# Kernel optimization log

Hardware: AMD Instinct MI355X
Metric: run time of the kernel (lower is better)

The kernel has to match this reference:

```python
import jax, jax.numpy as jnp
import numpy as np

H = 1024
B = 8
S = 2048

def setup_inputs() -> dict:
    key = jax.random.key(0)
    ks = jax.random.split(key, 16)
    w = lambda k, shp: (jax.random.normal(k, shp, dtype=jnp.float32) * 0.02)
    return {
        "hidden_states": jax.random.normal(ks[0], (B, S, H), dtype=jnp.float32),
        "context_vector": jax.random.normal(ks[1], (B, H), dtype=jnp.float32),
        # nn.Linear weights stored torch-style as [out, in]
        "Wq": w(ks[2], (H, H)), "bq": w(ks[3], (H,)),
        "Wk": w(ks[4], (H, H)), "bk": w(ks[5], (H,)),
        "Wv": w(ks[6], (H, H)), "bv": w(ks[7], (H,)),
        "Wcq": w(ks[8], (H, H)),  # only .weight.t() used in original (no bias)
        "Wck": w(ks[9], (H, H)),
        "g_qh": jax.random.normal(ks[10], (H, 1), dtype=jnp.float32),
        "g_kh": jax.random.normal(ks[11], (H, 1), dtype=jnp.float32),
        "g_qc": jax.random.normal(ks[12], (H, 1), dtype=jnp.float32),
        "g_kc": jax.random.normal(ks[13], (H, 1), dtype=jnp.float32),
    }

def reference(hidden_states, context_vector, Wq, bq, Wk, bk, Wv, bv, Wcq, Wck, g_qh, g_kh, g_qc, g_kc):
    # Linear projections (torch Linear: x @ W.T + b)
    query = jnp.einsum('bsh,oh->bso', hidden_states, Wq) + bq   # [B,S,H]
    key_  = jnp.einsum('bsh,oh->bso', hidden_states, Wk) + bk
    value = jnp.einsum('bsh,oh->bso', hidden_states, Wv) + bv

    # gate = sigmoid(Q @ g_h + (ctx @ g_c)[:,None,:])  -> [B,S,1]
    q_gate = jax.nn.sigmoid(query @ g_qh + (context_vector @ g_qc)[:, None, :])
    k_gate = jax.nn.sigmoid(key_  @ g_kh + (context_vector @ g_kc)[:, None, :])

    # context projections: ctx @ weight.t() (no bias in original usage) -> [B,1,H]
    ctx_q = (context_vector @ Wcq.T)[:, None, :]
    ctx_k = (context_vector @ Wck.T)[:, None, :]

    query_hat = (1.0 - q_gate) * query + q_gate * ctx_q
    key_hat   = (1.0 - k_gate) * key_  + k_gate * ctx_k

    scale = 1.0 / jnp.sqrt(jnp.asarray(H, dtype=jnp.float32))
    scores = jnp.einsum('bqh,bkh->bqk', query_hat, key_hat) * scale  # [B,S,S]
    probs = jax.nn.softmax(scores, axis=-1)
    output = jnp.einsum('bqk,bkh->bqh', probs, value)  # [B,S,H]
    return (output, scores)
```

## Files before the change

kernel.cpp:

```cpp
#include <hip/hip_runtime.h>
#include <cstdint>
#include <cstddef>

#define H 1024
#define NB 8
#define S 2048
#define MROWS (NB*S)

using short8  = __attribute__((ext_vector_type(8))) short;
using ushort8 = __attribute__((ext_vector_type(8))) unsigned short;
using f32x4   = __attribute__((ext_vector_type(4))) float;

__device__ __forceinline__ unsigned short f2bf(float f){
  union { float f; unsigned int u; } c; c.f = f;
  unsigned int u = c.u;
  return (unsigned short)((u + 0x7fffu + ((u >> 16) & 1u)) >> 16);
}
__device__ __forceinline__ float bf2f(unsigned short b){
  union { unsigned int u; float f; } c; c.u = ((unsigned int)b) << 16;
  return c.f;
}

__global__ __launch_bounds__(256) void k_prep(
    const float* __restrict__ Wq, const float* __restrict__ Wk, const float* __restrict__ Wv,
    const float* __restrict__ Wcq, const float* __restrict__ Wck, const float* __restrict__ ctx,
    const float* __restrict__ gqh, const float* __restrict__ gkh,
    const float* __restrict__ bq, const float* __restrict__ bk,
    const float* __restrict__ gqc, const float* __restrict__ gkc,
    unsigned short* __restrict__ wqb, unsigned short* __restrict__ wkb, unsigned short* __restrict__ wvb,
    float* __restrict__ up, float* __restrict__ ctxq, float* __restrict__ ctxk,
    float* __restrict__ scal)
{
  __shared__ float cs[NB * H];
  const int bid = blockIdx.x;
  const int t = threadIdx.x;
  if (bid < 3072){
    const int y = bid >> 10;
    const int x = bid & 1023;
    const float* src = y == 0 ? Wq : (y == 1 ? Wk : Wv);
    unsigned short* dst = y == 0 ? wqb : (y == 1 ? wkb : wvb);
    const int i = (x * 256 + t) * 4;
    float4 v = *reinterpret_cast<const float4*>(src + i);
    ushort4 o; o.x = f2bf(v.x); o.y = f2bf(v.y); o.z = f2bf(v.z); o.w = f2bf(v.w);
    *reinterpret_cast<ushort4*>(dst + i) = o;
  } else if (bid < 3136){
    const int sub = bid - 3072;
    const int z = sub >> 5;
    const int y = (sub >> 2) & 7;
    const int x = sub & 3;
    const float* W = z ? Wk : Wq;
    const float* g = z ? gkh : gqh;
    const int in = x * 256 + t;
    const int o0 = y * 128;
    float s = 0.f;
    for (int o = 0; o < 128; ++o) s = fmaf(W[(size_t)(o0 + o) * H + in], g[o0 + o], s);
    up[(z * 8 + y) * 1024 + in] = s;
  } else if (bid < 3648){
    const int sub = bid - 3136;
    const int y = sub >> 8;
    const int x = sub & 255;
    const float* W = y ? Wck : Wcq;
    float* out = y ? ctxk : ctxq;
    for (int i = t; i < NB * H; i += 256) cs[i] = ctx[i];
    __syncthreads();
    const int wid = t >> 6, lane = t & 63;
    const int row = x * 4 + wid;
    float a[NB];
    #pragma unroll
    for (int b = 0; b < NB; ++b) a[b] = 0.f;
    for (int i0 = 0; i0 < H; i0 += 64){
      const float w = W[(size_t)row * H + i0 + lane];
      #pragma unroll
      for (int b = 0; b < NB; ++b) a[b] = fmaf(w, cs[b * H + i0 + lane], a[b]);
    }
    #pragma unroll
    for (int b = 0; b < NB; ++b){
      float v = a[b];
      #pragma unroll
      for (int off = 32; off > 0; off >>= 1) v += __shfl_xor(v, off);
      if (lane == 0) out[b * H + row] = v;
    }
  } else {
    const int wid = t >> 6, lane = t & 63;
    for (int d = wid; d < 18; d += 4){
      const float *pa, *pb;
      if (d == 0){ pa = bq; pb = gqh; }
      else if (d == 1){ pa = bk; pb = gkh; }
      else if (d < 10){ pa = ctx + (d - 2) * H; pb = gqc; }
      else { pa = ctx + (d - 10) * H; pb = gkc; }
      float s = 0.f;
      for (int i = lane; i < H; i += 64) s = fmaf(pa[i], pb[i], s);
      #pragma unroll
      for (int off = 32; off > 0; off >>= 1) s += __shfl_xor(s, off);
      if (lane == 0) scal[d] = s;
    }
  }
}

__global__ void k_ucombine(const float* __restrict__ up, float* __restrict__ u2){
  int i = blockIdx.x * 256 + threadIdx.x;
  int z = i >> 10, h = i & 1023;
  float s = 0.f;
  #pragma unroll
  for (int c = 0; c < 8; ++c) s += up[(z * 8 + c) * 1024 + h];
  u2[i] = s;
}

__global__ __launch_bounds__(256) void k_prepass(const float* __restrict__ hs,
    const float* __restrict__ u2, const float* __restrict__ scal,
    unsigned short* __restrict__ hsb, float* __restrict__ gq, float* __restrict__ gk){
  const int t = threadIdx.x, wid = t >> 6, lane = t & 63;
  const int row = blockIdx.x * 4 + wid;
  const float* hrow = hs + (size_t)row * H;
  const float* u_q = u2;
  const float* u_k = u2 + 1024;
  unsigned short* orow = hsb + (size_t)row * H;
  float sq = 0.f, sk = 0.f;
  #pragma unroll
  for (int c = 0; c < 4; ++c){
    const int idx = (lane + c * 64) * 4;
    float4 v  = *reinterpret_cast<const float4*>(hrow + idx);
    float4 uq = *reinterpret_cast<const float4*>(u_q + idx);
    float4 uk = *reinterpret_cast<const float4*>(u_k + idx);
    ushort4 o; o.x = f2bf(v.x); o.y = f2bf(v.y); o.z = f2bf(v.z); o.w = f2bf(v.w);
    *reinterpret_cast<ushort4*>(orow + idx) = o;
    sq += v.x*uq.x + v.y*uq.y + v.z*uq.z + v.w*uq.w;
    sk += v.x*uk.x + v.y*uk.y + v.z*uk.z + v.w*uk.w;
  }
  #pragma unroll
  for (int off = 32; off > 0; off >>= 1){
    sq += __shfl_xor(sq, off);
    sk += __shfl_xor(sk, off);
  }
  if (lane == 0){
    const int b = row >> 11;
    gq[row] = 1.f / (1.f + __expf(-(sq + scal[0] + scal[2 + b])));
    gk[row] = 1.f / (1.f + __expf(-(sk + scal[1] + scal[10 + b])));
  }
}


#define STG(bufi, opi, halfi, koff, P0, P1) \
  do { __builtin_amdgcn_global_load_lds((const __attribute__((address_space(1))) void*)(P0 + (koff)), \
      (__attribute__((address_space(3))) void*)((char*)(&lds[bufi][opi][halfi][0]) + (wid*2+0)*1024), 16, 0, 0); \
    __builtin_amdgcn_global_load_lds((const __attribute__((address_space(1))) void*)(P1 + (koff)), \
      (__attribute__((address_space(3))) void*)((char*)(&lds[bufi][opi][halfi][0]) + (wid*2+1)*1024), 16, 0, 0); } while(0)
#define STG_A(bufi, halfi, koff) STG(bufi, 0, halfi, koff, sA0, sA1)
#define STG_B(bufi, halfi, koff) STG(bufi, 1, halfi, koff, sB0, sB1)

#define DS_A(bufi, ks, mh) \
  do { _Pragma("unroll") for (int m_ = 0; m_ < 4; ++m_){ \
      const int ar_ = wr*128 + ((mh)*4 + m_)*16 + (lane & 15); \
      const int sl_ = (lane >> 4) ^ ((ar_ >> 1) & 3); \
      af[m_] = *reinterpret_cast<const short8*>(&lds[bufi][0][ks][ar_*32 + sl_*8]); } } while(0)
#define DS_B(bufi, ks) \
  do { _Pragma("unroll") for (int n_ = 0; n_ < 4; ++n_){ \
      const int br_ = wc*64 + n_*16 + (lane & 15); \
      const int sl_ = (lane >> 4) ^ ((br_ >> 1) & 3); \
      bf[n_] = *reinterpret_cast<const short8*>(&lds[bufi][1][ks][br_*32 + sl_*8]); } } while(0)
#define MFMA16(mh) \
  do { __builtin_amdgcn_s_setprio(1); \
    _Pragma("unroll") for (int m_ = 0; m_ < 4; ++m_) \
      _Pragma("unroll") for (int n_ = 0; n_ < 4; ++n_) \
        acc[(mh)*4 + m_][n_] = __builtin_amdgcn_mfma_f32_16x16x32_bf16(af[m_], bf[n_], acc[(mh)*4 + m_][n_], 0, 0, 0); \
    __builtin_amdgcn_s_setprio(0); } while(0)
#define VM4() do { asm volatile("s_waitcnt vmcnt(4)" ::: "memory"); } while(0)
#define VM0() do { asm volatile("s_waitcnt vmcnt(0)" ::: "memory"); } while(0)
#define BAR() do { asm volatile("" ::: "memory"); __builtin_amdgcn_s_barrier(); asm volatile("" ::: "memory"); } while(0)

template<int MODE>
__global__ __launch_bounds__(512, 2)
void k_gemm(const unsigned short* __restrict__ A, const unsigned short* __restrict__ B,
            int K, int ldA, int ldB, long long Abatch, long long Bbatch,
            const float* __restrict__ gq, const float* __restrict__ gk,
            const float* __restrict__ bq, const float* __restrict__ bk, const float* __restrict__ bv,
            const float* __restrict__ cq, const float* __restrict__ ck,
            unsigned short* __restrict__ oq, unsigned short* __restrict__ ok, unsigned short* __restrict__ ov,
            float* __restrict__ outf, long long outBatch, float scale, float* __restrict__ rsum)
{
  __shared__ __align__(16) short lds[2][2][2][8192];

  const int t = threadIdx.x;
  const int wid = t >> 6, lane = t & 63;
  const int wr = wid >> 2, wc = wid & 3;
  const int bz = blockIdx.z;
  const unsigned short* Ab = A + (size_t)bz * (size_t)Abatch;
  const unsigned short* Bb = B + (size_t)bz * (size_t)Bbatch;
  const int row0 = blockIdx.x * 256;
  const int col0 = blockIdx.y * 256;

  const int c0 = (wid*2 + 0)*64 + lane;
  const int c1 = (wid*2 + 1)*64 + lane;
  const int r0s = c0 >> 2, r1s = c1 >> 2;
  const int kc0 = (c0 & 3) ^ ((r0s >> 1) & 3);
  const int kc1 = (c1 & 3) ^ ((r1s >> 1) & 3);
  const unsigned short* sA0 = Ab + (size_t)(row0 + r0s) * (size_t)ldA + kc0*8;
  const unsigned short* sA1 = Ab + (size_t)(row0 + r1s) * (size_t)ldA + kc1*8;
  const unsigned short* sB0 = Bb + (size_t)(col0 + r0s) * (size_t)ldB + kc0*8;
  const unsigned short* sB1 = Bb + (size_t)(col0 + r1s) * (size_t)ldB + kc1*8;

  f32x4 acc[8][4] = {};
  short8 af[4], bf[4];

  STG_A(0, 0, 0); STG_B(0, 0, 0); STG_A(0, 1, 32); STG_B(0, 1, 32);
  VM0(); BAR();

  const int niter = K >> 7;
  for (int it = 0; it < niter; ++it){
    const int t1k = (it*2 + 1) << 6;
    const int t2k = (it*2 + 2) << 6;
    const bool more = (it + 1 < niter);
    DS_A(0, 0, 0); DS_B(0, 0); STG_A(1, 0, t1k);      MFMA16(0);                              BAR();
    DS_A(0, 0, 1);             STG_B(1, 0, t1k);      MFMA16(1); VM4();                       BAR();
    DS_A(0, 1, 0); DS_B(0, 1); STG_A(1, 1, t1k + 32); MFMA16(0);                              BAR();
    DS_A(0, 1, 1);             STG_B(1, 1, t1k + 32); MFMA16(1); if (more) { VM4(); } else { VM0(); } BAR();
    DS_A(1, 0, 0); DS_B(1, 0); if (more) { STG_A(0, 0, t2k); }      MFMA16(0);                BAR();
    DS_A(1, 0, 1);             if (more) { STG_B(0, 0, t2k); }      MFMA16(1); if (more) { VM4(); } BAR();
    DS_A(1, 1, 0); DS_B(1, 1); if (more) { STG_A(0, 1, t2k + 32); } MFMA16(0);                BAR();
    DS_A(1, 1, 1);             if (more) { STG_B(0, 1, t2k + 32); } MFMA16(1); if (more) { VM4(); } BAR();
  }

  if constexpr (MODE == 0){
    const int which = col0 >> 10;
    const int lcol  = col0 & 1023;
    if (which < 2){
      const float* gate = which ? gk : gq;
      const float* bias = which ? bk : bq;
      const float* ctxv = which ? ck : cq;
      unsigned short* outb = which ? ok : oq;
      unsigned short* tp = (unsigned short*)lds;
      float* gl = (float*)((char*)lds + 69632);
      float* bl = gl + 256;
      float* cl = bl + 256;
      const int b = row0 >> 11;
      __syncthreads();
      if (t < 256){
        gl[t] = gate[row0 + t];
        bl[t] = bias[lcol + t];
        cl[t] = ctxv[b * H + lcol + t];
      }
      __syncthreads();
      #pragma unroll
      for (int ci = 0; ci < 2; ++ci){
        if (ci) __syncthreads();
        if (wr == ci){
          #pragma unroll
          for (int mi = 0; mi < 8; ++mi)
            #pragma unroll
            for (int r = 0; r < 4; ++r){
              const int lr = mi*16 + (lane >> 4)*4 + r;
              const float g = gl[ci*128 + lr];
              #pragma unroll
              for (int n = 0; n < 4; ++n){
                const int lc = wc*64 + n*16 + (lane & 15);
                const float q = acc[mi][n][r] + bl[lc];
                tp[lr*264 + lc] = f2bf((1.f - g) * q + g * cl[lc]);
              }
            }
        }
        __syncthreads();
        const int rr = t & 127;
        const int cc = (t >> 7) * 64;
        const unsigned short* srcp = tp + rr*264 + cc;
        unsigned short* dst = outb + (size_t)(row0 + ci*128 + rr) * H + lcol + cc;
        #pragma unroll
        for (int i = 0; i < 64; i += 8)
          *reinterpret_cast<ushort8*>(dst + i) = *reinterpret_cast<const ushort8*>(srcp + i);
      }
    } else {
      unsigned short* tp = (unsigned short*)lds;
      const int bb = row0 >> 11;
      const int s0 = row0 & (S - 1);
      #pragma unroll
      for (int ci = 0; ci < 2; ++ci)
        #pragma unroll
        for (int cj = 0; cj < 2; ++cj){
          __syncthreads();
          if (wr == ci && (wc >> 1) == cj){
            const int lc0 = (wc & 1) * 64;
            #pragma unroll
            for (int mi = 0; mi < 8; ++mi)
              #pragma unroll
              for (int n = 0; n < 4; ++n)
                #pragma unroll
                for (int r = 0; r < 4; ++r){
                  const int lr = mi*16 + (lane >> 4)*4 + r;
                  const int lc = lc0 + n*16 + (lane & 15);
                  tp[lc*136 + lr] = f2bf(acc[mi][n][r] + bv[lcol + cj*128 + lc]);
                }
          }
          __syncthreads();
          const int hh = t & 127;
          const int sc = (t >> 7) * 32;
          const unsigned short* srcp = tp + hh*136 + sc;
          unsigned short* vout = ov + (size_t)bb * H * S + (size_t)(lcol + cj*128 + hh) * S
                                    + (size_t)(s0 + ci*128 + sc);
          #pragma unroll
          for (int i2 = 0; i2 < 32; i2 += 8)
            *reinterpret_cast<ushort8*>(vout + i2) = *reinterpret_cast<const ushort8*>(srcp + i2);
        }
    }
  } else if constexpr (MODE == 3){
    float* rowacc = (float*)lds;
    __syncthreads();
    if (t < 256) rowacc[t] = 0.f;
    __syncthreads();
    #pragma unroll
    for (int mi = 0; mi < 8; ++mi)
      #pragma unroll
      for (int r = 0; r < 4; ++r){
        const int lr = wr*128 + mi*16 + (lane >> 4)*4 + r;
        const int grow = row0 + lr;
        float psum = 0.f;
        #pragma unroll
        for (int n = 0; n < 4; ++n){
          const int gcol = col0 + wc*64 + n*16 + (lane & 15);
          const float val = acc[mi][n][r] * scale;
          outf[(size_t)bz * (size_t)outBatch + (size_t)grow * S + gcol] = val;
          const float pe = __expf(fminf(val, 80.f));
          const unsigned short pb = f2bf(pe);
          oq[(size_t)bz * (size_t)outBatch + (size_t)grow * S + gcol] = pb;
          psum += bf2f(pb);
        }
        #pragma unroll
        for (int off = 1; off < 16; off <<= 1) psum += __shfl_xor(psum, off);
        if ((lane & 15) == 0) atomicAdd(&rowacc[lr], psum);
      }
    __syncthreads();
    if (t < 256) atomicAdd(&rsum[bz * S + row0 + t], rowacc[t]);
  } else {
    float* rs = (float*)lds;
    __syncthreads();
    if (t < 256) rs[t] = 1.f / fmaxf(rsum[bz * S + row0 + t], 1e-35f);
    __syncthreads();
    #pragma unroll
    for (int mi = 0; mi < 8; ++mi)
      #pragma unroll
      for (int r = 0; r < 4; ++r){
        const int lr = wr*128 + mi*16 + (lane >> 4)*4 + r;
        const float inv = rs[lr];
        #pragma unroll
        for (int n = 0; n < 4; ++n){
          const int gcol = col0 + wc*64 + n*16 + (lane & 15);
          outf[(size_t)bz * (size_t)outBatch + (size_t)(row0 + lr) * H + gcol] = acc[mi][n][r] * inv;
        }
      }
  }
}

extern "C" void kernel_launch(void* const* d_in, const int* in_sizes, int n_in,
                              void* d_out, int out_size, void* d_ws, size_t ws_size,
                              hipStream_t stream) {
  const float* hs  = (const float*)d_in[0];
  const float* ctx = (const float*)d_in[1];
  const float* Wq  = (const float*)d_in[2];
  const float* bq  = (const float*)d_in[3];
  const float* Wk  = (const float*)d_in[4];
  const float* bk  = (const float*)d_in[5];
  const float* Wv  = (const float*)d_in[6];
  const float* bv  = (const float*)d_in[7];
  const float* Wcq = (const float*)d_in[8];
  const float* Wck = (const float*)d_in[9];
  const float* gqh = (const float*)d_in[10];
  const float* gkh = (const float*)d_in[11];
  const float* gqc = (const float*)d_in[12];
  const float* gkc = (const float*)d_in[13];

  char* ws = (char*)d_ws;
  unsigned short* hsb   = (unsigned short*)(ws);
  unsigned short* qhat  = (unsigned short*)(ws + 33554432);
  unsigned short* khat  = (unsigned short*)(ws + 67108864);
  unsigned short* vt    = (unsigned short*)(ws + 100663296);
  unsigned short* probs = (unsigned short*)(ws + 134217728);
  unsigned short* wqb   = (unsigned short*)(ws + 201326592);
  unsigned short* wkb   = (unsigned short*)(ws + 203423744);
  unsigned short* wvb   = (unsigned short*)(ws + 205520896);
  float* up    = (float*)(ws + 207618048);
  float* u2    = (float*)(ws + 207683584);
  float* ctxq  = (float*)(ws + 207691776);
  float* ctxk  = (float*)(ws + 207724544);
  float* gq    = (float*)(ws + 207757312);
  float* gk    = (float*)(ws + 207822848);
  float* scal  = (float*)(ws + 207888384);
  float* rsum  = (float*)(ws + 207888640);

  float* out_attn   = (float*)d_out;
  float* out_scores = out_attn + (size_t)MROWS * H;

  hipMemsetAsync(rsum, 0, MROWS * sizeof(float), stream);

  k_prep<<<3649, 256, 0, stream>>>(Wq, Wk, Wv, Wcq, Wck, ctx, gqh, gkh, bq, bk, gqc, gkc,
      wqb, wkb, wvb, up, ctxq, ctxk, scal);
  k_ucombine<<<8, 256, 0, stream>>>(up, u2);
  k_prepass<<<MROWS / 4, 256, 0, stream>>>(hs, u2, scal, hsb, gq, gk);

  k_gemm<0><<<dim3(64, 12, 1), 512, 0, stream>>>(hsb, wqb, 1024, 1024, 1024, 0, 0,
      gq, gk, bq, bk, bv, ctxq, ctxk, qhat, khat, vt, nullptr, 0, 1.f, nullptr);

  k_gemm<3><<<dim3(8, 8, 8), 512, 0, stream>>>(qhat, khat, 1024, 1024, 1024,
      (long long)S * H, (long long)S * H,
      nullptr, nullptr, nullptr, nullptr, nullptr, nullptr, nullptr,
      probs, nullptr, nullptr, out_scores, (long long)S * S, 0.03125f, rsum);

  k_gemm<5><<<dim3(8, 4, 8), 512, 0, stream>>>(probs, vt, 2048, 2048, 2048,
      (long long)S * S, (long long)H * S,
      nullptr, nullptr, nullptr, nullptr, nullptr, nullptr, nullptr,
      nullptr, nullptr, nullptr, out_attn, (long long)S * H, 1.f, rsum);
}
```

Before: 327.6 us.

## Shrink GEMM tiles to 128x128 with 256 threads and single-buffered LDS

Replaces the 256x256-tile, 512-thread, double-buffered software-pipelined GEMM with a 128x128-tile, 256-thread kernel. The new kernel loads a 64-wide K slice per iteration, waits, then computes. It uses less LDS and fewer registers so three blocks can fit per CU, and launches four times as many blocks. In exchange it loses the overlap between global-to-LDS loads and MFMA work, and it halves operand reuse per tile, which raises global and L2 traffic. The epilogues are simplified to match the smaller tile.

```diff
diff --git a/kernel.cpp b/kernel.cpp
--- a/kernel.cpp
+++ b/kernel.cpp
@@ -140,36 +140,11 @@
 }
 
 
-#define STG(bufi, opi, halfi, koff, P0, P1) \
-  do { __builtin_amdgcn_global_load_lds((const __attribute__((address_space(1))) void*)(P0 + (koff)), \
-      (__attribute__((address_space(3))) void*)((char*)(&lds[bufi][opi][halfi][0]) + (wid*2+0)*1024), 16, 0, 0); \
-    __builtin_amdgcn_global_load_lds((const __attribute__((address_space(1))) void*)(P1 + (koff)), \
-      (__attribute__((address_space(3))) void*)((char*)(&lds[bufi][opi][halfi][0]) + (wid*2+1)*1024), 16, 0, 0); } while(0)
-#define STG_A(bufi, halfi, koff) STG(bufi, 0, halfi, koff, sA0, sA1)
-#define STG_B(bufi, halfi, koff) STG(bufi, 1, halfi, koff, sB0, sB1)
-
-#define DS_A(bufi, ks, mh) \
-  do { _Pragma("unroll") for (int m_ = 0; m_ < 4; ++m_){ \
-      const int ar_ = wr*128 + ((mh)*4 + m_)*16 + (lane & 15); \
-      const int sl_ = (lane >> 4) ^ ((ar_ >> 1) & 3); \
-      af[m_] = *reinterpret_cast<const short8*>(&lds[bufi][0][ks][ar_*32 + sl_*8]); } } while(0)
-#define DS_B(bufi, ks) \
-  do { _Pragma("unroll") for (int n_ = 0; n_ < 4; ++n_){ \
-      const int br_ = wc*64 + n_*16 + (lane & 15); \
-      const int sl_ = (lane >> 4) ^ ((br_ >> 1) & 3); \
-      bf[n_] = *reinterpret_cast<const short8*>(&lds[bufi][1][ks][br_*32 + sl_*8]); } } while(0)
-#define MFMA16(mh) \
-  do { __builtin_amdgcn_s_setprio(1); \
-    _Pragma("unroll") for (int m_ = 0; m_ < 4; ++m_) \
-      _Pragma("unroll") for (int n_ = 0; n_ < 4; ++n_) \
-        acc[(mh)*4 + m_][n_] = __builtin_amdgcn_mfma_f32_16x16x32_bf16(af[m_], bf[n_], acc[(mh)*4 + m_][n_], 0, 0, 0); \
-    __builtin_amdgcn_s_setprio(0); } while(0)
-#define VM4() do { asm volatile("s_waitcnt vmcnt(4)" ::: "memory"); } while(0)
 #define VM0() do { asm volatile("s_waitcnt vmcnt(0)" ::: "memory"); } while(0)
 #define BAR() do { asm volatile("" ::: "memory"); __builtin_amdgcn_s_barrier(); asm volatile("" ::: "memory"); } while(0)
 
 template<int MODE>
-__global__ __launch_bounds__(512, 2)
+__global__ __launch_bounds__(256, 3)
 void k_gemm(const unsigned short* __restrict__ A, const unsigned short* __restrict__ B,
             int K, int ldA, int ldB, long long Abatch, long long Bbatch,
             const float* __restrict__ gq, const float* __restrict__ gk,
@@ -178,46 +153,69 @@
             unsigned short* __restrict__ oq, unsigned short* __restrict__ ok, unsigned short* __restrict__ ov,
             float* __restrict__ outf, long long outBatch, float scale, float* __restrict__ rsum)
 {
-  __shared__ __align__(16) short lds[2][2][2][8192];
+  __shared__ __align__(16) short lds[20480];
+  short* As = lds;
+  short* Bs = lds + 8192;
 
   const int t = threadIdx.x;
   const int wid = t >> 6, lane = t & 63;
-  const int wr = wid >> 2, wc = wid & 3;
+  const int wr = wid >> 1, wc = wid & 1;
   const int bz = blockIdx.z;
   const unsigned short* Ab = A + (size_t)bz * (size_t)Abatch;
   const unsigned short* Bb = B + (size_t)bz * (size_t)Bbatch;
-  const int row0 = blockIdx.x * 256;
-  const int col0 = blockIdx.y * 256;
-
-  const int c0 = (wid*2 + 0)*64 + lane;
-  const int c1 = (wid*2 + 1)*64 + lane;
-  const int r0s = c0 >> 2, r1s = c1 >> 2;
-  const int kc0 = (c0 & 3) ^ ((r0s >> 1) & 3);
-  const int kc1 = (c1 & 3) ^ ((r1s >> 1) & 3);
-  const unsigned short* sA0 = Ab + (size_t)(row0 + r0s) * (size_t)ldA + kc0*8;
-  const unsigned short* sA1 = Ab + (size_t)(row0 + r1s) * (size_t)ldA + kc1*8;
-  const unsigned short* sB0 = Bb + (size_t)(col0 + r0s) * (size_t)ldB + kc0*8;
-  const unsigned short* sB1 = Bb + (size_t)(col0 + r1s) * (size_t)ldB + kc1*8;
-
-  f32x4 acc[8][4] = {};
+  const int row0 = blockIdx.x * 128;
+  const int col0 = blockIdx.y * 128;
+
+  const unsigned short* srcA[4];
+  const unsigned short* srcB[4];
+  #pragma unroll
+  for (int i = 0; i < 4; ++i){
+    const int c = (wid*4 + i)*64 + lane;
+    const int r = c >> 3, sl = c & 7;
+    const int kcg = sl ^ (r & 7);
+    srcA[i] = Ab + (size_t)(row0 + r) * (size_t)ldA + kcg*8;
+    srcB[i] = Bb + (size_t)(col0 + r) * (size_t)ldB + kcg*8;
+  }
+
+  f32x4 acc[4][4] = {};
   short8 af[4], bf[4];
 
-  STG_A(0, 0, 0); STG_B(0, 0, 0); STG_A(0, 1, 32); STG_B(0, 1, 32);
-  VM0(); BAR();
-
-  const int niter = K >> 7;
-  for (int it = 0; it < niter; ++it){
-    const int t1k = (it*2 + 1) << 6;
-    const int t2k = (it*2 + 2) << 6;
-    const bool more = (it + 1 < niter);
-    DS_A(0, 0, 0); DS_B(0, 0); STG_A(1, 0, t1k);      MFMA16(0);                              BAR();
-    DS_A(0, 0, 1);             STG_B(1, 0, t1k);      MFMA16(1); VM4();                       BAR();
-    DS_A(0, 1, 0); DS_B(0, 1); STG_A(1, 1, t1k + 32); MFMA16(0);                              BAR();
-    DS_A(0, 1, 1);             STG_B(1, 1, t1k + 32); MFMA16(1); if (more) { VM4(); } else { VM0(); } BAR();
-    DS_A(1, 0, 0); DS_B(1, 0); if (more) { STG_A(0, 0, t2k); }      MFMA16(0);                BAR();
-    DS_A(1, 0, 1);             if (more) { STG_B(0, 0, t2k); }      MFMA16(1); if (more) { VM4(); } BAR();
-    DS_A(1, 1, 0); DS_B(1, 1); if (more) { STG_A(0, 1, t2k + 32); } MFMA16(0);                BAR();
-    DS_A(1, 1, 1);             if (more) { STG_B(0, 1, t2k + 32); } MFMA16(1); if (more) { VM4(); } BAR();
+  const int nkt = K >> 6;
+  for (int kt = 0; kt < nkt; ++kt){
+    const int k0 = kt << 6;
+    #pragma unroll
+    for (int i = 0; i < 4; ++i){
+      __builtin_amdgcn_global_load_lds(
+        (const __attribute__((address_space(1))) void*)(srcA[i] + k0),
+        (__attribute__((address_space(3))) void*)((char*)As + (wid*4 + i)*1024), 16, 0, 0);
+      __builtin_amdgcn_global_load_lds(
+        (const __attribute__((address_space(1))) void*)(srcB[i] + k0),
+        (__attribute__((address_space(3))) void*)((char*)Bs + (wid*4 + i)*1024), 16, 0, 0);
+    }
+    VM0(); BAR();
+    #pragma unroll
+    for (int kk = 0; kk < 2; ++kk){
+      #pragma unroll
+      for (int m = 0; m < 4; ++m){
+        const int ar = wr*64 + m*16 + (lane & 15);
+        const int ssl = (kk*4 + (lane >> 4)) ^ (ar & 7);
+        af[m] = *reinterpret_cast<const short8*>(&As[ar*64 + ssl*8]);
+      }
+      #pragma unroll
+      for (int n = 0; n < 4; ++n){
+        const int br = wc*64 + n*16 + (lane & 15);
+        const int ssl = (kk*4 + (lane >> 4)) ^ (br & 7);
+        bf[n] = *reinterpret_cast<const short8*>(&Bs[br*64 + ssl*8]);
+      }
+      __builtin_amdgcn_s_setprio(1);
+      #pragma unroll
+      for (int m = 0; m < 4; ++m)
+        #pragma unroll
+        for (int n = 0; n < 4; ++n)
+          acc[m][n] = __builtin_amdgcn_mfma_f32_16x16x32_bf16(af[m], bf[n], acc[m][n], 0, 0, 0);
+      __builtin_amdgcn_s_setprio(0);
+    }
+    BAR();
   }
 
   if constexpr (MODE == 0){
@@ -229,93 +227,79 @@
       const float* ctxv = which ? ck : cq;
       unsigned short* outb = which ? ok : oq;
       unsigned short* tp = (unsigned short*)lds;
-      float* gl = (float*)((char*)lds + 69632);
-      float* bl = gl + 256;
-      float* cl = bl + 256;
+      float* gl = (float*)((char*)lds + 34816);
+      float* bl = gl + 128;
+      float* cl = bl + 128;
       const int b = row0 >> 11;
       __syncthreads();
-      if (t < 256){
+      if (t < 128){
         gl[t] = gate[row0 + t];
         bl[t] = bias[lcol + t];
         cl[t] = ctxv[b * H + lcol + t];
       }
       __syncthreads();
       #pragma unroll
-      for (int ci = 0; ci < 2; ++ci){
-        if (ci) __syncthreads();
-        if (wr == ci){
+      for (int m = 0; m < 4; ++m)
+        #pragma unroll
+        for (int r = 0; r < 4; ++r){
+          const int lr = wr*64 + m*16 + (lane >> 4)*4 + r;
+          const float g = gl[lr];
           #pragma unroll
-          for (int mi = 0; mi < 8; ++mi)
-            #pragma unroll
-            for (int r = 0; r < 4; ++r){
-              const int lr = mi*16 + (lane >> 4)*4 + r;
-              const float g = gl[ci*128 + lr];
-              #pragma unroll
-              for (int n = 0; n < 4; ++n){
-                const int lc = wc*64 + n*16 + (lane & 15);
-                const float q = acc[mi][n][r] + bl[lc];
-                tp[lr*264 + lc] = f2bf((1.f - g) * q + g * cl[lc]);
-              }
-            }
+          for (int n = 0; n < 4; ++n){
+            const int lc = wc*64 + n*16 + (lane & 15);
+            const float q = acc[m][n][r] + bl[lc];
+            tp[lr*136 + lc] = f2bf((1.f - g) * q + g * cl[lc]);
+          }
         }
-        __syncthreads();
-        const int rr = t & 127;
-        const int cc = (t >> 7) * 64;
-        const unsigned short* srcp = tp + rr*264 + cc;
-        unsigned short* dst = outb + (size_t)(row0 + ci*128 + rr) * H + lcol + cc;
-        #pragma unroll
-        for (int i = 0; i < 64; i += 8)
-          *reinterpret_cast<ushort8*>(dst + i) = *reinterpret_cast<const ushort8*>(srcp + i);
-      }
+      __syncthreads();
+      const int rr = t & 127;
+      const int cc = (t >> 7) * 64;
+      const unsigned short* srcp = tp + rr*136 + cc;
+      unsigned short* dst = outb + (size_t)(row0 + rr) * H + lcol + cc;
+      #pragma unroll
+      for (int i = 0; i < 64; i += 8)
+        *reinterpret_cast<ushort8*>(dst + i) = *reinterpret_cast<const ushort8*>(srcp + i);
     } else {
       unsigned short* tp = (unsigned short*)lds;
       const int bb = row0 >> 11;
       const int s0 = row0 & (S - 1);
-      #pragma unroll
-      for (int ci = 0; ci < 2; ++ci)
-        #pragma unroll
-        for (int cj = 0; cj < 2; ++cj){
-          __syncthreads();
-          if (wr == ci && (wc >> 1) == cj){
-            const int lc0 = (wc & 1) * 64;
-            #pragma unroll
-            for (int mi = 0; mi < 8; ++mi)
-              #pragma unroll
-              for (int n = 0; n < 4; ++n)
-                #pragma unroll
-                for (int r = 0; r < 4; ++r){
-                  const int lr = mi*16 + (lane >> 4)*4 + r;
-                  const int lc = lc0 + n*16 + (lane & 15);
-                  tp[lc*136 + lr] = f2bf(acc[mi][n][r] + bv[lcol + cj*128 + lc]);
-                }
+      __syncthreads();
+      #pragma unroll
+      for (int m = 0; m < 4; ++m)
+        #pragma unroll
+        for (int r = 0; r < 4; ++r){
+          const int lr = wr*64 + m*16 + (lane >> 4)*4 + r;
+          #pragma unroll
+          for (int n = 0; n < 4; ++n){
+            const int lc = wc*64 + n*16 + (lane & 15);
+            tp[lc*136 + lr] = f2bf(acc[m][n][r] + bv[lcol + lc]);
           }
-          __syncthreads();
-          const int hh = t & 127;
-          const int sc = (t >> 7) * 32;
-          const unsigned short* srcp = tp + hh*136 + sc;
-          unsigned short* vout = ov + (size_t)bb * H * S + (size_t)(lcol + cj*128 + hh) * S
-                                    + (size_t)(s0 + ci*128 + sc);
-          #pragma unroll
-          for (int i2 = 0; i2 < 32; i2 += 8)
-            *reinterpret_cast<ushort8*>(vout + i2) = *reinterpret_cast<const ushort8*>(srcp + i2);
         }
+      __syncthreads();
+      const int hh = t & 127;
+      const int sc = (t >> 7) * 64;
+      const unsigned short* srcp = tp + hh*136 + sc;
+      unsigned short* vout = ov + (size_t)bb * H * S + (size_t)(lcol + hh) * S + (size_t)(s0 + sc);
+      #pragma unroll
+      for (int i = 0; i < 64; i += 8)
+        *reinterpret_cast<ushort8*>(vout + i) = *reinterpret_cast<const ushort8*>(srcp + i);
     }
   } else if constexpr (MODE == 3){
     float* rowacc = (float*)lds;
     __syncthreads();
-    if (t < 256) rowacc[t] = 0.f;
-    __syncthreads();
-    #pragma unroll
-    for (int mi = 0; mi < 8; ++mi)
+    if (t < 128) rowacc[t] = 0.f;
+    __syncthreads();
+    #pragma unroll
+    for (int m = 0; m < 4; ++m)
       #pragma unroll
       for (int r = 0; r < 4; ++r){
-        const int lr = wr*128 + mi*16 + (lane >> 4)*4 + r;
+        const int lr = wr*64 + m*16 + (lane >> 4)*4 + r;
         const int grow = row0 + lr;
         float psum = 0.f;
         #pragma unroll
         for (int n = 0; n < 4; ++n){
           const int gcol = col0 + wc*64 + n*16 + (lane & 15);
-          const float val = acc[mi][n][r] * scale;
+          const float val = acc[m][n][r] * scale;
           outf[(size_t)bz * (size_t)outBatch + (size_t)grow * S + gcol] = val;
           const float pe = __expf(fminf(val, 80.f));
           const unsigned short pb = f2bf(pe);
@@ -327,22 +311,22 @@
         if ((lane & 15) == 0) atomicAdd(&rowacc[lr], psum);
       }
     __syncthreads();
-    if (t < 256) atomicAdd(&rsum[bz * S + row0 + t], rowacc[t]);
+    if (t < 128) atomicAdd(&rsum[bz * S + row0 + t], rowacc[t]);
   } else {
     float* rs = (float*)lds;
     __syncthreads();
-    if (t < 256) rs[t] = 1.f / fmaxf(rsum[bz * S + row0 + t], 1e-35f);
-    __syncthreads();
-    #pragma unroll
-    for (int mi = 0; mi < 8; ++mi)
+    if (t < 128) rs[t] = 1.f / fmaxf(rsum[bz * S + row0 + t], 1e-35f);
+    __syncthreads();
+    #pragma unroll
+    for (int m = 0; m < 4; ++m)
       #pragma unroll
       for (int r = 0; r < 4; ++r){
-        const int lr = wr*128 + mi*16 + (lane >> 4)*4 + r;
+        const int lr = wr*64 + m*16 + (lane >> 4)*4 + r;
         const float inv = rs[lr];
         #pragma unroll
         for (int n = 0; n < 4; ++n){
           const int gcol = col0 + wc*64 + n*16 + (lane & 15);
-          outf[(size_t)bz * (size_t)outBatch + (size_t)(row0 + lr) * H + gcol] = acc[mi][n][r] * inv;
+          outf[(size_t)bz * (size_t)outBatch + (size_t)(row0 + lr) * H + gcol] = acc[m][n][r] * inv;
         }
       }
   }
@@ -394,15 +378,15 @@
   k_ucombine<<<8, 256, 0, stream>>>(up, u2);
   k_prepass<<<MROWS / 4, 256, 0, stream>>>(hs, u2, scal, hsb, gq, gk);
 
-  k_gemm<0><<<dim3(64, 12, 1), 512, 0, stream>>>(hsb, wqb, 1024, 1024, 1024, 0, 0,
+  k_gemm<0><<<dim3(128, 24, 1), 256, 0, stream>>>(hsb, wqb, 1024, 1024, 1024, 0, 0,
       gq, gk, bq, bk, bv, ctxq, ctxk, qhat, khat, vt, nullptr, 0, 1.f, nullptr);
 
-  k_gemm<3><<<dim3(8, 8, 8), 512, 0, stream>>>(qhat, khat, 1024, 1024, 1024,
+  k_gemm<3><<<dim3(16, 16, 8), 256, 0, stream>>>(qhat, khat, 1024, 1024, 1024,
       (long long)S * H, (long long)S * H,
       nullptr, nullptr, nullptr, nullptr, nullptr, nullptr, nullptr,
       probs, nullptr, nullptr, out_scores, (long long)S * S, 0.03125f, rsum);
 
-  k_gemm<5><<<dim3(8, 4, 8), 512, 0, stream>>>(probs, vt, 2048, 2048, 2048,
+  k_gemm<5><<<dim3(16, 8, 8), 256, 0, stream>>>(probs, vt, 2048, 2048, 2048,
       (long long)S * S, (long long)H * S,
       nullptr, nullptr, nullptr, nullptr, nullptr, nullptr, nullptr,
       nullptr, nullptr, nullptr, out_attn, (long long)S * H, 1.f, rsum);
```

New measurement: 343.8 us. 4.9% more time.
